# Kernel tuning notes

Measured on AMD Instinct MI355X. Metric: run time of the kernel, lower is better.

## Reference

```python
import jax, jax.numpy as jnp
import numpy as np

B, C, L = 256, 500, 200
D, H, NUM_ITEMS = 64, 128, 100000
BETA = 0.7
EPS = 1e-8


def _xavier(key, fan_in, fan_out):
    lim = float(np.sqrt(6.0 / (fan_in + fan_out)))
    return jax.random.uniform(key, (fan_in, fan_out), minval=-lim, maxval=lim, dtype=jnp.float32)


def setup_inputs() -> dict:
    key = jax.random.key(0)
    ks = jax.random.split(key, 12)
    inp = {
        'candidate_items': jax.random.randint(ks[0], (B, C), 0, NUM_ITEMS, dtype=jnp.int64) if jax.config.read('jax_enable_x64') else jax.random.randint(ks[0], (B, C), 0, NUM_ITEMS),
        'query_times': jax.random.uniform(ks[1], (B,), dtype=jnp.float32),
        'candidate_histories': jax.random.uniform(ks[2], (B, C, L), dtype=jnp.float32),
        'item_emb': 0.02 * jax.random.normal(ks[3], (NUM_ITEMS, D), dtype=jnp.float32),
        'base_W1': _xavier(ks[4], D, H), 'base_b1': jnp.zeros((H,), jnp.float32),
        'base_W2': _xavier(ks[5], H, H), 'base_b2': jnp.zeros((H,), jnp.float32),
        'base_W3': _xavier(ks[6], H, 1),
        'exc_W1': _xavier(ks[7], D, H), 'exc_b1': jnp.zeros((H,), jnp.float32),
        'exc_W2': _xavier(ks[8], H, H), 'exc_b2': jnp.zeros((H,), jnp.float32),
        'exc_W3': _xavier(ks[9], H, 1),
    }
    return inp


def _mlp(x, W1, b1, W2, b2, W3):
    # (Linear + Softplus) x depth, then Linear -> 1 (no bias), squeeze last dim
    h = jax.nn.softplus(x @ W1 + b1)
    h = jax.nn.softplus(h @ W2 + b2)
    return (h @ W3)[..., 0]


def reference(candidate_items, query_times, candidate_histories, item_emb,
              base_W1, base_b1, base_W2, base_b2, base_W3,
              exc_W1, exc_b1, exc_W2, exc_b2, exc_W3):
    z = item_emb[candidate_items]                                  # [B, C, D]
    mu = jax.nn.softplus(_mlp(z, base_W1, base_b1, base_W2, base_b2, base_W3)) + EPS   # [B, C]
    alpha = jax.nn.softplus(_mlp(z, exc_W1, exc_b1, exc_W2, exc_b2, exc_W3)) + EPS     # [B, C]
    q = query_times[:, None, None]                                 # [B, 1, 1]
    mask = candidate_histories < q                                 # [B, C, L]
    delta = jnp.maximum(q - candidate_histories, 0.0)              # clamp(min=0)
    h = jnp.sum(jnp.exp(-BETA * delta) * mask, axis=-1)            # [B, C]
    return mu + alpha * h
```

## Files before the change

### kernel.cpp

```cpp
#include <hip/hip_runtime.h>
#include <math.h>

#define BB 256
#define CC 500
#define LL 200
#define DD 64
#define HH 128
#define NUM_ITEMS 100000
#define BETA 0.7f
#define EPSV 1e-8f

#define TM 32
#define WPB 4
#define IPB (TM * WPB)
#define NBLK ((NUM_ITEMS + IPB - 1) / IPB)

typedef _Float16 half8 __attribute__((ext_vector_type(8)));
typedef float floatx4 __attribute__((ext_vector_type(4)));

__device__ __forceinline__ float softplus_f(float x) {
    float t = __expf(-fabsf(x));
    return fmaxf(x, 0.0f) + __logf(1.0f + t);
}

__global__ __launch_bounds__(256) void prep_w(
    const float* __restrict__ W1, const float* __restrict__ W2,
    const float* __restrict__ V1, const float* __restrict__ V2,
    _Float16* __restrict__ wb)
{
    int t = blockIdx.x * 256 + threadIdx.x;
    if (t >= 49152) return;
    float v;
    if (t < 8192)       { int n = t >> 6,  k = t & 63;             v = W1[k * HH + n]; }
    else if (t < 24576) { int u = t - 8192;  int n = u >> 7, k = u & 127; v = W2[k * HH + n]; }
    else if (t < 32768) { int u = t - 24576; int n = u >> 6, k = u & 63;  v = V1[k * HH + n]; }
    else                { int u = t - 32768; int n = u >> 7, k = u & 127; v = V2[k * HH + n]; }
    wb[t] = (_Float16)v;
}

__global__ __launch_bounds__(256) void mlp_mfma(
    const float* __restrict__ emb, const _Float16* __restrict__ wb,
    const float* __restrict__ b1, const float* __restrict__ b2, const float* __restrict__ W3,
    const float* __restrict__ c1, const float* __restrict__ c2, const float* __restrict__ V3,
    float* __restrict__ mu, float* __restrict__ alpha)
{
    __shared__ _Float16 h1s[WPB][TM * 136];
    int tid  = threadIdx.x;
    int wave = tid >> 6, lane = tid & 63;
    int quad = lane >> 4, l15 = lane & 15;

    int is_exc = blockIdx.x >= NBLK;
    int blk    = blockIdx.x - (is_exc ? NBLK : 0);
    int ibase  = blk * IPB + wave * TM;

    const _Float16* W1t = wb + (is_exc ? 24576 : 0);
    const _Float16* W2t = wb + (is_exc ? 32768 : 8192);
    const float* B1 = is_exc ? c1 : b1;
    const float* B2 = is_exc ? c2 : b2;
    const float* W3p = is_exc ? V3 : W3;
    float* outp = is_exc ? alpha : mu;
    _Float16* hs = &h1s[wave][0];

    half8 zf[2][2];
    #pragma unroll
    for (int mt = 0; mt < 2; ++mt) {
        int item = ibase + mt * 16 + l15;
        int src = item < NUM_ITEMS ? item : NUM_ITEMS - 1;
        const float* p = emb + (size_t)src * DD + quad * 8;
        #pragma unroll
        for (int kt = 0; kt < 2; ++kt) {
            floatx4 v0 = *(const floatx4*)(p + kt * 32);
            floatx4 v1 = *(const floatx4*)(p + kt * 32 + 4);
            half8 z;
            #pragma unroll
            for (int j = 0; j < 4; ++j) { z[j] = (_Float16)v0[j]; z[4 + j] = (_Float16)v1[j]; }
            zf[mt][kt] = z;
        }
    }

    #pragma unroll
    for (int h = 0; h < 2; ++h) {
        floatx4 acc[2][4];
        #pragma unroll
        for (int n = 0; n < 4; ++n) {
            float bv = B1[(h * 4 + n) * 16 + l15];
            #pragma unroll
            for (int mt = 0; mt < 2; ++mt) acc[mt][n] = (floatx4){bv, bv, bv, bv};
        }
        half8 wf[4][2];
        #pragma unroll
        for (int n = 0; n < 4; ++n)
            #pragma unroll
            for (int kt = 0; kt < 2; ++kt)
                wf[n][kt] = *(const half8*)(W1t + ((h * 4 + n) * 16 + l15) * DD + kt * 32 + quad * 8);
        #pragma unroll
        for (int kt = 0; kt < 2; ++kt)
            #pragma unroll
            for (int n = 0; n < 4; ++n)
                #pragma unroll
                for (int mt = 0; mt < 2; ++mt)
                    acc[mt][n] = __builtin_amdgcn_mfma_f32_16x16x32_f16(zf[mt][kt], wf[n][kt], acc[mt][n], 0, 0, 0);
        #pragma unroll
        for (int mt = 0; mt < 2; ++mt)
            #pragma unroll
            for (int n = 0; n < 4; ++n)
                #pragma unroll
                for (int r = 0; r < 4; ++r) {
                    int it = mt * 16 + quad * 4 + r;
                    int j  = (h * 4 + n) * 16 + l15;
                    hs[it * 136 + j] = (_Float16)softplus_f(acc[mt][n][r]);
                }
    }
    __syncthreads();

    float sacc[2][4];
    #pragma unroll
    for (int mt = 0; mt < 2; ++mt)
        #pragma unroll
        for (int r = 0; r < 4; ++r) sacc[mt][r] = 0.0f;

    #pragma unroll
    for (int h = 0; h < 2; ++h) {
        floatx4 acc[2][4];
        #pragma unroll
        for (int n = 0; n < 4; ++n) {
            float bv = B2[(h * 4 + n) * 16 + l15];
            #pragma unroll
            for (int mt = 0; mt < 2; ++mt) acc[mt][n] = (floatx4){bv, bv, bv, bv};
        }
        #pragma unroll
        for (int kt = 0; kt < 4; ++kt) {
            half8 af[2];
            #pragma unroll
            for (int mt = 0; mt < 2; ++mt)
                af[mt] = *(const half8*)(hs + (mt * 16 + l15) * 136 + kt * 32 + quad * 8);
            half8 wf[4];
            #pragma unroll
            for (int n = 0; n < 4; ++n)
                wf[n] = *(const half8*)(W2t + ((h * 4 + n) * 16 + l15) * HH + kt * 32 + quad * 8);
            #pragma unroll
            for (int n = 0; n < 4; ++n)
                #pragma unroll
                for (int mt = 0; mt < 2; ++mt)
                    acc[mt][n] = __builtin_amdgcn_mfma_f32_16x16x32_f16(af[mt], wf[n], acc[mt][n], 0, 0, 0);
        }
        #pragma unroll
        for (int n = 0; n < 4; ++n) {
            float w3 = W3p[(h * 4 + n) * 16 + l15];
            #pragma unroll
            for (int mt = 0; mt < 2; ++mt)
                #pragma unroll
                for (int r = 0; r < 4; ++r)
                    sacc[mt][r] += softplus_f(acc[mt][n][r]) * w3;
        }
    }
    #pragma unroll
    for (int mt = 0; mt < 2; ++mt)
        #pragma unroll
        for (int r = 0; r < 4; ++r) {
            float s = sacc[mt][r];
            s += __shfl_xor(s, 1, 64);
            s += __shfl_xor(s, 2, 64);
            s += __shfl_xor(s, 4, 64);
            s += __shfl_xor(s, 8, 64);
            if (l15 == 0) {
                int item = ibase + mt * 16 + quad * 4 + r;
                if (item < NUM_ITEMS) outp[item] = softplus_f(s) + EPSV;
            }
        }
}

__global__ __launch_bounds__(256) void hawkes_kernel(
    const int* __restrict__ items,
    const float* __restrict__ qt,
    const float* __restrict__ hist,
    const float* __restrict__ mu,
    const float* __restrict__ alpha,
    float* __restrict__ out)
{
    int w = blockIdx.x * 4 + (threadIdx.x >> 6);
    int lane = threadIdx.x & 63;
    float q = qt[w / CC];

    float s = 0.0f;
    if (lane < LL / 4) {
        float4 v = *(const float4*)(hist + (size_t)w * LL + lane * 4);
        s  = (v.x < q) ? __expf(BETA * v.x) : 0.f;
        s += (v.y < q) ? __expf(BETA * v.y) : 0.f;
        s += (v.z < q) ? __expf(BETA * v.z) : 0.f;
        s += (v.w < q) ? __expf(BETA * v.w) : 0.f;
    }
    #pragma unroll
    for (int off = 1; off < 64; off <<= 1) s += __shfl_xor(s, off, 64);

    if (lane == 0) {
        int it = items[w];
        out[w] = fmaf(alpha[it] * __expf(-BETA * q), s, mu[it]);
    }
}

extern "C" void kernel_launch(void* const* d_in, const int* in_sizes, int n_in,
                              void* d_out, int out_size, void* d_ws, size_t ws_size,
                              hipStream_t stream)
{
    const int*   items = (const int*)  d_in[0];
    const float* qt    = (const float*)d_in[1];
    const float* hist  = (const float*)d_in[2];
    const float* emb   = (const float*)d_in[3];
    const float* W1    = (const float*)d_in[4];
    const float* b1    = (const float*)d_in[5];
    const float* W2    = (const float*)d_in[6];
    const float* b2    = (const float*)d_in[7];
    const float* W3    = (const float*)d_in[8];
    const float* V1    = (const float*)d_in[9];
    const float* c1    = (const float*)d_in[10];
    const float* V2    = (const float*)d_in[11];
    const float* c2    = (const float*)d_in[12];
    const float* V3    = (const float*)d_in[13];

    float* out = (float*)d_out;
    _Float16* wb = (_Float16*)d_ws;
    float* mu    = (float*)((char*)d_ws + 98304);
    float* alpha = mu + NUM_ITEMS;

    prep_w<<<192, 256, 0, stream>>>(W1, W2, V1, V2, wb);

    mlp_mfma<<<2 * NBLK, 256, 0, stream>>>(emb, wb, b1, b2, W3, c1, c2, V3, mu, alpha);

    hawkes_kernel<<<(BB * CC) / 4, 256, 0, stream>>>(items, qt, hist, mu, alpha, out);
}
```

Measured before the change: 260.8 us.

## Make MLP kernel persistent with register-resident weights and prefetched embeddings

The MLP kernel becomes persistent: a fixed set of 1024 waves per MLP loops over 32-item tiles with a grid stride. Each wave loads all W1/W2 fragments, biases and W3 into registers once, and the next tile's embeddings are prefetched during the current tile's compute. The inner softplus switches to an unguarded log(1+exp(x)) form, which could overflow for large inputs. Register pressure rises sharply (launch bounds 128,1), which lowers occupancy. The syncthreads is dropped because each wave uses only its own shared slice.

```diff
diff --git a/kernel.cpp b/kernel.cpp
--- a/kernel.cpp
+++ b/kernel.cpp
@@ -11,16 +11,19 @@
 #define EPSV 1e-8f
 
 #define TM 32
-#define WPB 4
-#define IPB (TM * WPB)
-#define NBLK ((NUM_ITEMS + IPB - 1) / IPB)
+#define WPB 2
+#define NTILE (NUM_ITEMS / TM)
+#define NWSET 1024
 
 typedef _Float16 half8 __attribute__((ext_vector_type(8)));
 typedef float floatx4 __attribute__((ext_vector_type(4)));
 
-__device__ __forceinline__ float softplus_f(float x) {
+__device__ __forceinline__ float softplus_safe(float x) {
     float t = __expf(-fabsf(x));
     return fmaxf(x, 0.0f) + __logf(1.0f + t);
+}
+__device__ __forceinline__ float softplus_fast(float x) {
+    return __logf(1.0f + __expf(x));
 }
 
 __global__ __launch_bounds__(256) void prep_w(
@@ -38,136 +41,158 @@
     wb[t] = (_Float16)v;
 }
 
-__global__ __launch_bounds__(256) void mlp_mfma(
+__device__ __forceinline__ void prefetch_z(const float* __restrict__ emb, int t,
+                                           int l15, int quad, floatx4 (&zraw)[2][2][2]) {
+    #pragma unroll
+    for (int mt = 0; mt < 2; ++mt) {
+        const float* p = emb + (size_t)(t * TM + mt * 16 + l15) * DD + quad * 8;
+        #pragma unroll
+        for (int kt = 0; kt < 2; ++kt) {
+            zraw[mt][kt][0] = *(const floatx4*)(p + kt * 32);
+            zraw[mt][kt][1] = *(const floatx4*)(p + kt * 32 + 4);
+        }
+    }
+}
+
+__global__ __launch_bounds__(128, 1) void mlp_mfma(
     const float* __restrict__ emb, const _Float16* __restrict__ wb,
     const float* __restrict__ b1, const float* __restrict__ b2, const float* __restrict__ W3,
     const float* __restrict__ c1, const float* __restrict__ c2, const float* __restrict__ V3,
     float* __restrict__ mu, float* __restrict__ alpha)
 {
-    __shared__ _Float16 h1s[WPB][TM * 136];
+    __shared__ _Float16 h1s[WPB * TM * 136];
     int tid  = threadIdx.x;
     int wave = tid >> 6, lane = tid & 63;
     int quad = lane >> 4, l15 = lane & 15;
 
-    int is_exc = blockIdx.x >= NBLK;
-    int blk    = blockIdx.x - (is_exc ? NBLK : 0);
-    int ibase  = blk * IPB + wave * TM;
+    int wid    = blockIdx.x * WPB + wave;
+    int is_exc = wid >= NWSET;
+    int wslot  = wid & (NWSET - 1);
 
     const _Float16* W1t = wb + (is_exc ? 24576 : 0);
     const _Float16* W2t = wb + (is_exc ? 32768 : 8192);
-    const float* B1 = is_exc ? c1 : b1;
-    const float* B2 = is_exc ? c2 : b2;
+    const float* B1  = is_exc ? c1 : b1;
+    const float* B2  = is_exc ? c2 : b2;
     const float* W3p = is_exc ? V3 : W3;
     float* outp = is_exc ? alpha : mu;
-    _Float16* hs = &h1s[wave][0];
-
-    half8 zf[2][2];
+    _Float16* hs = h1s + wave * TM * 136;
+
+    half8 w1f[2][2][4];
+    half8 w2f[2][4][4];
+    float b1v[2][4], b2v[2][4], w3v[2][4];
     #pragma unroll
-    for (int mt = 0; mt < 2; ++mt) {
-        int item = ibase + mt * 16 + l15;
-        int src = item < NUM_ITEMS ? item : NUM_ITEMS - 1;
-        const float* p = emb + (size_t)src * DD + quad * 8;
-        #pragma unroll
-        for (int kt = 0; kt < 2; ++kt) {
-            floatx4 v0 = *(const floatx4*)(p + kt * 32);
-            floatx4 v1 = *(const floatx4*)(p + kt * 32 + 4);
-            half8 z;
-            #pragma unroll
-            for (int j = 0; j < 4; ++j) { z[j] = (_Float16)v0[j]; z[4 + j] = (_Float16)v1[j]; }
-            zf[mt][kt] = z;
-        }
-    }
-
-    #pragma unroll
-    for (int h = 0; h < 2; ++h) {
-        floatx4 acc[2][4];
+    for (int h = 0; h < 2; ++h)
         #pragma unroll
         for (int n = 0; n < 4; ++n) {
-            float bv = B1[(h * 4 + n) * 16 + l15];
-            #pragma unroll
-            for (int mt = 0; mt < 2; ++mt) acc[mt][n] = (floatx4){bv, bv, bv, bv};
-        }
-        half8 wf[4][2];
-        #pragma unroll
-        for (int n = 0; n < 4; ++n)
+            int j = (h * 4 + n) * 16 + l15;
+            b1v[h][n] = B1[j];
+            b2v[h][n] = B2[j];
+            w3v[h][n] = W3p[j];
             #pragma unroll
             for (int kt = 0; kt < 2; ++kt)
-                wf[n][kt] = *(const half8*)(W1t + ((h * 4 + n) * 16 + l15) * DD + kt * 32 + quad * 8);
-        #pragma unroll
-        for (int kt = 0; kt < 2; ++kt)
-            #pragma unroll
-            for (int n = 0; n < 4; ++n)
+                w1f[h][kt][n] = *(const half8*)(W1t + j * DD + kt * 32 + quad * 8);
+            #pragma unroll
+            for (int kt = 0; kt < 4; ++kt)
+                w2f[h][kt][n] = *(const half8*)(W2t + j * HH + kt * 32 + quad * 8);
+        }
+
+    floatx4 zraw[2][2][2];
+    prefetch_z(emb, wslot, l15, quad, zraw);
+
+    #pragma unroll 1
+    for (int t = wslot; t < NTILE; t += NWSET) {
+        half8 zf[2][2];
+        #pragma unroll
+        for (int mt = 0; mt < 2; ++mt)
+            #pragma unroll
+            for (int kt = 0; kt < 2; ++kt) {
+                half8 z;
+                #pragma unroll
+                for (int j = 0; j < 4; ++j) {
+                    z[j]     = (_Float16)zraw[mt][kt][0][j];
+                    z[4 + j] = (_Float16)zraw[mt][kt][1][j];
+                }
+                zf[mt][kt] = z;
+            }
+        int tn = (t + NWSET < NTILE) ? t + NWSET : t;
+        prefetch_z(emb, tn, l15, quad, zraw);
+
+        #pragma unroll
+        for (int h = 0; h < 2; ++h) {
+            floatx4 acc[2][4];
+            #pragma unroll
+            for (int n = 0; n < 4; ++n) {
+                float bv = b1v[h][n];
+                #pragma unroll
+                for (int mt = 0; mt < 2; ++mt) acc[mt][n] = (floatx4){bv, bv, bv, bv};
+            }
+            #pragma unroll
+            for (int kt = 0; kt < 2; ++kt)
+                #pragma unroll
+                for (int n = 0; n < 4; ++n)
+                    #pragma unroll
+                    for (int mt = 0; mt < 2; ++mt)
+                        acc[mt][n] = __builtin_amdgcn_mfma_f32_16x16x32_f16(zf[mt][kt], w1f[h][kt][n], acc[mt][n], 0, 0, 0);
+            #pragma unroll
+            for (int mt = 0; mt < 2; ++mt)
+                #pragma unroll
+                for (int n = 0; n < 4; ++n)
+                    #pragma unroll
+                    for (int r = 0; r < 4; ++r)
+                        hs[(mt * 16 + quad * 4 + r) * 136 + (h * 4 + n) * 16 + l15] =
+                            (_Float16)softplus_fast(acc[mt][n][r]);
+        }
+
+        float sacc[2][4];
+        #pragma unroll
+        for (int mt = 0; mt < 2; ++mt)
+            #pragma unroll
+            for (int r = 0; r < 4; ++r) sacc[mt][r] = 0.0f;
+
+        #pragma unroll
+        for (int h = 0; h < 2; ++h) {
+            floatx4 acc[2][4];
+            #pragma unroll
+            for (int n = 0; n < 4; ++n) {
+                float bv = b2v[h][n];
+                #pragma unroll
+                for (int mt = 0; mt < 2; ++mt) acc[mt][n] = (floatx4){bv, bv, bv, bv};
+            }
+            #pragma unroll
+            for (int kt = 0; kt < 4; ++kt) {
+                half8 af[2];
                 #pragma unroll
                 for (int mt = 0; mt < 2; ++mt)
-                    acc[mt][n] = __builtin_amdgcn_mfma_f32_16x16x32_f16(zf[mt][kt], wf[n][kt], acc[mt][n], 0, 0, 0);
+                    af[mt] = *(const half8*)(hs + (mt * 16 + l15) * 136 + kt * 32 + quad * 8);
+                #pragma unroll
+                for (int n = 0; n < 4; ++n)
+                    #pragma unroll
+                    for (int mt = 0; mt < 2; ++mt)
+                        acc[mt][n] = __builtin_amdgcn_mfma_f32_16x16x32_f16(af[mt], w2f[h][kt][n], acc[mt][n], 0, 0, 0);
+            }
+            #pragma unroll
+            for (int n = 0; n < 4; ++n) {
+                float w3 = w3v[h][n];
+                #pragma unroll
+                for (int mt = 0; mt < 2; ++mt)
+                    #pragma unroll
+                    for (int r = 0; r < 4; ++r)
+                        sacc[mt][r] += softplus_fast(acc[mt][n][r]) * w3;
+            }
+        }
         #pragma unroll
         for (int mt = 0; mt < 2; ++mt)
             #pragma unroll
-            for (int n = 0; n < 4; ++n)
-                #pragma unroll
-                for (int r = 0; r < 4; ++r) {
-                    int it = mt * 16 + quad * 4 + r;
-                    int j  = (h * 4 + n) * 16 + l15;
-                    hs[it * 136 + j] = (_Float16)softplus_f(acc[mt][n][r]);
-                }
-    }
-    __syncthreads();
-
-    float sacc[2][4];
-    #pragma unroll
-    for (int mt = 0; mt < 2; ++mt)
-        #pragma unroll
-        for (int r = 0; r < 4; ++r) sacc[mt][r] = 0.0f;
-
-    #pragma unroll
-    for (int h = 0; h < 2; ++h) {
-        floatx4 acc[2][4];
-        #pragma unroll
-        for (int n = 0; n < 4; ++n) {
-            float bv = B2[(h * 4 + n) * 16 + l15];
-            #pragma unroll
-            for (int mt = 0; mt < 2; ++mt) acc[mt][n] = (floatx4){bv, bv, bv, bv};
-        }
-        #pragma unroll
-        for (int kt = 0; kt < 4; ++kt) {
-            half8 af[2];
-            #pragma unroll
-            for (int mt = 0; mt < 2; ++mt)
-                af[mt] = *(const half8*)(hs + (mt * 16 + l15) * 136 + kt * 32 + quad * 8);
-            half8 wf[4];
-            #pragma unroll
-            for (int n = 0; n < 4; ++n)
-                wf[n] = *(const half8*)(W2t + ((h * 4 + n) * 16 + l15) * HH + kt * 32 + quad * 8);
-            #pragma unroll
-            for (int n = 0; n < 4; ++n)
-                #pragma unroll
-                for (int mt = 0; mt < 2; ++mt)
-                    acc[mt][n] = __builtin_amdgcn_mfma_f32_16x16x32_f16(af[mt], wf[n], acc[mt][n], 0, 0, 0);
-        }
-        #pragma unroll
-        for (int n = 0; n < 4; ++n) {
-            float w3 = W3p[(h * 4 + n) * 16 + l15];
-            #pragma unroll
-            for (int mt = 0; mt < 2; ++mt)
-                #pragma unroll
-                for (int r = 0; r < 4; ++r)
-                    sacc[mt][r] += softplus_f(acc[mt][n][r]) * w3;
-        }
-    }
-    #pragma unroll
-    for (int mt = 0; mt < 2; ++mt)
-        #pragma unroll
-        for (int r = 0; r < 4; ++r) {
-            float s = sacc[mt][r];
-            s += __shfl_xor(s, 1, 64);
-            s += __shfl_xor(s, 2, 64);
-            s += __shfl_xor(s, 4, 64);
-            s += __shfl_xor(s, 8, 64);
-            if (l15 == 0) {
-                int item = ibase + mt * 16 + quad * 4 + r;
-                if (item < NUM_ITEMS) outp[item] = softplus_f(s) + EPSV;
-            }
-        }
+            for (int r = 0; r < 4; ++r) {
+                float s = sacc[mt][r];
+                s += __shfl_xor(s, 1, 64);
+                s += __shfl_xor(s, 2, 64);
+                s += __shfl_xor(s, 4, 64);
+                s += __shfl_xor(s, 8, 64);
+                if (l15 == 0)
+                    outp[t * TM + mt * 16 + quad * 4 + r] = softplus_safe(s) + EPSV;
+            }
+    }
 }
 
 __global__ __launch_bounds__(256) void hawkes_kernel(
@@ -225,7 +250,7 @@
 
     prep_w<<<192, 256, 0, stream>>>(W1, W2, V1, V2, wb);
 
-    mlp_mfma<<<2 * NBLK, 256, 0, stream>>>(emb, wb, b1, b2, W3, c1, c2, V3, mu, alpha);
+    mlp_mfma<<<2 * NWSET / WPB, WPB * 64, 0, stream>>>(emb, wb, b1, b2, W3, c1, c2, V3, mu, alpha);
 
     hawkes_kernel<<<(BB * CC) / 4, 256, 0, stream>>>(items, qt, hist, mu, alpha, out);
 }
```

Measured after the change: 256.7 us. Within noise of the previous version (-1.6%).
